# Kernel optimization log

Measured on AMD Instinct MI355X. Metric: run time of the kernel, lower is better.

Reference implementation:

```python
import jax, jax.numpy as jnp
import numpy as np

NEG = -1000000000.0
EPS = 1e-05

def setup_inputs() -> dict:
    key = jax.random.key(0)
    k1, k2, k3, k4, k5 = jax.random.split(key, 5)
    B, L, E, Q = 64, 2048, 512, 256
    encoded_vecs = jax.random.normal(k1, (B, L, E), dtype=jnp.float32)
    query = jax.random.normal(k2, (B, Q), dtype=jnp.float32)
    length = jax.random.randint(k3, (B,), 1, L + 1, dtype=jnp.int32)
    # Xavier-normal-ish params
    W1 = jax.random.normal(k4, (E + Q, E), dtype=jnp.float32) * jnp.sqrt(2.0 / (E + Q + E))
    b1 = jnp.zeros((E,), dtype=jnp.float32)
    v = jax.random.normal(k5, (E,), dtype=jnp.float32) * jnp.sqrt(2.0 / (E + 1))
    return {"encoded_vecs": encoded_vecs, "query": query, "length": length,
            "W1": W1, "b1": b1, "v": v}

def reference(encoded_vecs, query, length, W1, b1, v):
    B, L, E = encoded_vecs.shape
    # broadcast 2D query over the length dim (repeat in torch code)
    q = jnp.broadcast_to(query[:, None, :], (B, L, query.shape[-1]))
    h = jnp.concatenate([encoded_vecs, q], axis=2)            # [B, L, E+Q]
    u = jnp.tanh(jnp.einsum('blc,ce->ble', h, W1) + b1)       # [B, L, E]
    logits = jnp.einsum('ble,e->bl', u, v)                    # [B, L]
    # masked softmax (faithful to masked_softmax in source)
    mask = (jnp.arange(L)[None, :] < length[:, None])         # [B, L] bool
    masked_logits = jnp.where(mask, logits, NEG)
    max_logits = jnp.max(masked_logits, axis=1, keepdims=True)
    exps = jnp.exp(masked_logits - max_logits) * mask.astype(logits.dtype)
    attention = exps / (jnp.sum(exps, axis=1, keepdims=True) + EPS)  # [B, L]
    context = jnp.einsum('bl,ble->be', attention, encoded_vecs)      # [B, E]
    return (context, attention)
```

## Files before the change

kernel.cpp:

```cpp
#include <hip/hip_runtime.h>

typedef __attribute__((ext_vector_type(4))) float float4v;
typedef __attribute__((ext_vector_type(2))) float float2v;
typedef __attribute__((ext_vector_type(8))) short short8;
typedef __attribute__((ext_vector_type(4))) float f32x4;

#define NEGV (-1000000000.0f)

#define MTOT (64 * 2048)

__device__ __forceinline__ unsigned short f2bf(float f) {
    unsigned int u = __float_as_uint(f);
    u += 0x7fffu + ((u >> 16) & 1u);
    return (unsigned short)(u >> 16);
}

__device__ __forceinline__ void gload_lds16(const void* g, void* l) {
    __builtin_amdgcn_global_load_lds(
        (__attribute__((address_space(1))) unsigned int*)(unsigned long long)(g),
        (__attribute__((address_space(3))) unsigned int*)(unsigned int)(unsigned long long)(l),
        16, 0, 0);
}

__global__ __launch_bounds__(256)
void prep_wt_kernel(const float* __restrict__ W1, unsigned short* __restrict__ Wt) {
    __shared__ float t[32][33];
    int bx = blockIdx.x & 15;
    int by = blockIdx.x >> 4;
    int tx = threadIdx.x & 31;
    int ty = threadIdx.x >> 5;
    #pragma unroll
    for (int i = 0; i < 4; ++i)
        t[ty + 8 * i][tx] = W1[(bx * 32 + ty + 8 * i) * 512 + by * 32 + tx];
    __syncthreads();
    #pragma unroll
    for (int i = 0; i < 4; ++i)
        Wt[(by * 32 + ty + 8 * i) * 512 + bx * 32 + tx] = f2bf(t[tx][ty + 8 * i]);
}

__global__ void prep_qc_kernel(const float* __restrict__ query, const float* __restrict__ W1,
                               const float* __restrict__ b1, float* __restrict__ qc) {
    int b = blockIdx.x;
    int e = threadIdx.x;
    float acc0 = b1[e];
    float acc1 = b1[e + 256];
    const float* w = W1 + 512 * 512;
    #pragma unroll 8
    for (int q = 0; q < 256; ++q) {
        float qv = query[b * 256 + q];
        acc0 += qv * w[q * 512 + e];
        acc1 += qv * w[q * 512 + e + 256];
    }
    qc[b * 512 + e] = acc0;
    qc[b * 512 + e + 256] = acc1;
}

__global__ __launch_bounds__(256)
void prep_enc_kernel(const float* __restrict__ enc, const int* __restrict__ length,
                     unsigned short* __restrict__ Ab) {
    int bm = blockIdx.x;
    int b = bm >> 4;
    if ((bm & 15) * 128 >= length[b]) return;
    long base = (long)bm * 128 * 512;
    const float* src = enc + base;
    unsigned short* dst = Ab + base;
    int tid = threadIdx.x;
    #pragma unroll 4
    for (int i = 0; i < 32; ++i) {
        long idx = (long)(i * 256 + tid) * 8;
        float4v a = *(const float4v*)(src + idx);
        float4v c = *(const float4v*)(src + idx + 4);
        union { unsigned short u[8]; short8 s; } o;
        o.u[0] = f2bf(a[0]); o.u[1] = f2bf(a[1]); o.u[2] = f2bf(a[2]); o.u[3] = f2bf(a[3]);
        o.u[4] = f2bf(c[0]); o.u[5] = f2bf(c[1]); o.u[6] = f2bf(c[2]); o.u[7] = f2bf(c[3]);
        *(short8*)(dst + idx) = o.s;
    }
}

__global__ void build_wl_kernel(const int* __restrict__ length, int* __restrict__ wl,
                                int* __restrict__ meta) {
    int bm = blockIdx.x * 256 + threadIdx.x;
    int b = bm >> 4;
    if ((bm & 15) * 128 < length[b]) {
        int idx = atomicAdd(&meta[0], 1);
        wl[idx] = bm;
    }
}

__global__ __launch_bounds__(512)
void gemm_logits_kernel(const unsigned short* __restrict__ Ab,
                        const unsigned short* __restrict__ Wt,
                        const float* __restrict__ qc,
                        const float* __restrict__ v,
                        const int* __restrict__ wl,
                        int* __restrict__ meta,
                        float* __restrict__ part)
{
    __shared__ unsigned short As[3 * 128 * 64];
    __shared__ unsigned short Bs[3 * 256 * 64];
    __shared__ int s_t;

    int tid = threadIdx.x;
    int lane = tid & 63;
    int w = tid >> 6;
    int wm = w >> 2, wn = w & 3;

    int aoffs[2], boffs[4];
    int asrc[2], bsrc[4];
    #pragma unroll
    for (int i = 0; i < 2; ++i) {
        int off = (w * 2 + i) * 1024 + lane * 16;
        int r = off >> 7, kb = off & 127;
        aoffs[i] = off;
        asrc[i] = r * 1024 + (kb ^ ((r & 7) << 4));
    }
    #pragma unroll
    for (int i = 0; i < 4; ++i) {
        int off = (w * 4 + i) * 1024 + lane * 16;
        int r = off >> 7, kb = off & 127;
        boffs[i] = off;
        bsrc[i] = r * 1024 + (kb ^ ((r & 7) << 4));
    }

    int aoff[4][2], boff[4][2];
    int kbase = (lane >> 4) * 16;
    #pragma unroll
    for (int mi = 0; mi < 4; ++mi) {
        int ar = wm * 64 + (lane & 15) + mi * 16;
        #pragma unroll
        for (int kk = 0; kk < 2; ++kk)
            aoff[mi][kk] = ar * 128 + ((kk * 64 + kbase) ^ ((ar & 7) << 4));
    }
    #pragma unroll
    for (int ni = 0; ni < 4; ++ni) {
        int br = wn * 64 + (lane & 15) + ni * 16;
        #pragma unroll
        for (int kk = 0; kk < 2; ++kk)
            boff[ni][kk] = br * 128 + ((kk * 64 + kbase) ^ ((br & 7) << 4));
    }

    int nw = meta[0] * 2;

    for (;;) {
        if (tid == 0) s_t = atomicAdd(&meta[1], 1);
        __syncthreads();
        int t = s_t;
        if (t >= nw) break;
        int bm = wl[t >> 1];
        int bn = t & 1;
        int b = bm >> 4;
        long row0 = (long)bm * 128;
        int col0 = bn * 256;

        const char* gA = (const char*)Ab + row0 * 1024;
        const char* gB = (const char*)Wt + (long)col0 * 1024;

        f32x4 acc[4][4] = {};

#define STAGE(t_, sI) do {                                                   \
    char* la_ = (char*)As + (sI) * 16384;                                    \
    char* lb_ = (char*)Bs + (sI) * 32768;                                    \
    gload_lds16(gA + asrc[0] + (t_) * 128, la_ + aoffs[0]);                  \
    gload_lds16(gA + asrc[1] + (t_) * 128, la_ + aoffs[1]);                  \
    gload_lds16(gB + bsrc[0] + (t_) * 128, lb_ + boffs[0]);                  \
    gload_lds16(gB + bsrc[1] + (t_) * 128, lb_ + boffs[1]);                  \
    gload_lds16(gB + bsrc[2] + (t_) * 128, lb_ + boffs[2]);                  \
    gload_lds16(gB + bsrc[3] + (t_) * 128, lb_ + boffs[3]);                  \
} while (0)

#define KCOMP(sC) do {                                                       \
    const char* as_ = (const char*)As + (sC) * 16384;                        \
    const char* bs_ = (const char*)Bs + (sC) * 32768;                        \
    _Pragma("unroll")                                                        \
    for (int kk = 0; kk < 2; ++kk) {                                         \
        short8 af_[4];                                                       \
        _Pragma("unroll")                                                    \
        for (int mi = 0; mi < 4; ++mi)                                       \
            af_[mi] = *(const short8*)(as_ + aoff[mi][kk]);                  \
        _Pragma("unroll")                                                    \
        for (int ni = 0; ni < 4; ++ni) {                                     \
            short8 bf_ = *(const short8*)(bs_ + boff[ni][kk]);               \
            _Pragma("unroll")                                                \
            for (int mi = 0; mi < 4; ++mi)                                   \
                acc[mi][ni] = __builtin_amdgcn_mfma_f32_16x16x32_bf16(af_[mi], bf_, acc[mi][ni], 0, 0, 0); \
        }                                                                    \
    }                                                                        \
} while (0)

#define KITER(t_, stg_, sI_, sC_, VM_) do {                                  \
    STAGE(stg_, sI_);                                                        \
    asm volatile("s_waitcnt vmcnt(" #VM_ ")" ::: "memory");                  \
    __builtin_amdgcn_s_barrier();                                            \
    asm volatile("" ::: "memory");                                           \
    KCOMP(sC_);                                                              \
    asm volatile("" ::: "memory");                                           \
    __builtin_amdgcn_s_barrier();                                            \
} while (0)

        STAGE(0, 0);
        STAGE(1, 1);
        KITER(0, 2, 2, 0, 12);
        KITER(1, 3, 0, 1, 12);
        KITER(2, 4, 1, 2, 12);
        KITER(3, 5, 2, 0, 12);
        KITER(4, 6, 0, 1, 12);
        KITER(5, 7, 1, 2, 12);
        asm volatile("s_waitcnt vmcnt(6)" ::: "memory");
        __builtin_amdgcn_s_barrier();
        asm volatile("" ::: "memory");
        KCOMP(0);
        asm volatile("" ::: "memory");
        __builtin_amdgcn_s_barrier();
        asm volatile("s_waitcnt vmcnt(0)" ::: "memory");
        __builtin_amdgcn_s_barrier();
        asm volatile("" ::: "memory");
        KCOMP(1);

        const float* qcb = qc + b * 512;
        float vcol[4], qcol[4];
        #pragma unroll
        for (int ni = 0; ni < 4; ++ni) {
            int c = col0 + wn * 64 + ni * 16 + (lane & 15);
            vcol[ni] = v[c];
            qcol[ni] = qcb[c];
        }
        float* pslice = part + (bn * 4 + wn) * MTOT + row0;
        int rbase = wm * 64 + 4 * (lane >> 4);
        #pragma unroll
        for (int mi = 0; mi < 4; ++mi) {
            #pragma unroll
            for (int j2 = 0; j2 < 4; ++j2) {
                float s = 0.f;
                #pragma unroll
                for (int ni = 0; ni < 4; ++ni) {
                    float xx = acc[mi][ni][j2] + qcol[ni];
                    float e2 = __expf(2.0f * xx);
                    float tt = 1.0f - 2.0f * __builtin_amdgcn_rcpf(e2 + 1.0f);
                    s += tt * vcol[ni];
                }
                s += __shfl_xor(s, 1);
                s += __shfl_xor(s, 2);
                s += __shfl_xor(s, 4);
                s += __shfl_xor(s, 8);
                if ((lane & 15) == 0)
                    pslice[rbase + mi * 16 + j2] = s;
            }
        }
    }
}

__global__ void softmax_kernel(const float* __restrict__ part, const int* __restrict__ length,
                               float* __restrict__ att, float* __restrict__ ctx) {
    int b = blockIdx.x;
    int len = length[b];
    int tid = threadIdx.x;
    int lane = tid & 63, wv = tid >> 6;
    const float* p0 = part + b * 2048;
    float* ab = att + b * 2048;

    ctx[b * 512 + tid] = 0.f;
    ctx[b * 512 + 256 + tid] = 0.f;

    float vals[8];
    float mymax = -3.402823466e38f;
    #pragma unroll
    for (int i = 0; i < 8; ++i) {
        int l = tid + i * 256;
        float xv = NEGV;
        if (l < len) {
            xv = 0.f;
            #pragma unroll
            for (int s = 0; s < 8; ++s)
                xv += p0[s * MTOT + l];
        }
        vals[i] = xv;
        mymax = fmaxf(mymax, xv);
    }
    #pragma unroll
    for (int m = 32; m; m >>= 1) mymax = fmaxf(mymax, __shfl_xor(mymax, m));
    __shared__ float sm[4];
    if (lane == 0) sm[wv] = mymax;
    __syncthreads();
    float bmax = fmaxf(fmaxf(sm[0], sm[1]), fmaxf(sm[2], sm[3]));

    float mysum = 0.f;
    #pragma unroll
    for (int i = 0; i < 8; ++i) {
        int l = tid + i * 256;
        float e = (l < len) ? __expf(vals[i] - bmax) : 0.f;
        vals[i] = e;
        mysum += e;
    }
    #pragma unroll
    for (int m = 32; m; m >>= 1) mysum += __shfl_xor(mysum, m);
    __shared__ float ss[4];
    if (lane == 0) ss[wv] = mysum;
    __syncthreads();
    float tot = ss[0] + ss[1] + ss[2] + ss[3];
    float inv = 1.0f / (tot + 1e-5f);
    #pragma unroll
    for (int i = 0; i < 8; ++i) {
        int l = tid + i * 256;
        ab[l] = vals[i] * inv;
    }
}

__global__ void ctx_kernel(const float* __restrict__ att, const unsigned short* __restrict__ Ab,
                           const int* __restrict__ length, float* __restrict__ ctx) {
    int b = blockIdx.x;
    int lc = blockIdx.y;
    int len = length[b];
    int l0 = lc * 128;
    if (l0 >= len) return;
    int lim = len - l0;
    if (lim > 128) lim = 128;

    int t = threadIdx.x;
    const float* ab = att + b * 2048 + l0;
    const unsigned short* eb = Ab + ((long)(b * 2048 + l0)) * 512 + t * 2;
    float c0 = 0.f, c1 = 0.f;
    #pragma unroll 4
    for (int l = 0; l < lim; ++l) {
        float a = ab[l];
        unsigned int wv = *(const unsigned int*)(eb);
        eb += 512;
        c0 += a * __uint_as_float(wv << 16);
        c1 += a * __uint_as_float(wv & 0xffff0000u);
    }
    atomicAdd(&ctx[b * 512 + 2 * t], c0);
    atomicAdd(&ctx[b * 512 + 2 * t + 1], c1);
}

extern "C" void kernel_launch(void* const* d_in, const int* in_sizes, int n_in,
                              void* d_out, int out_size, void* d_ws, size_t ws_size,
                              hipStream_t stream) {
    const float* enc    = (const float*)d_in[0];
    const float* query  = (const float*)d_in[1];
    const int*   length = (const int*)d_in[2];
    const float* W1     = (const float*)d_in[3];
    const float* b1     = (const float*)d_in[4];
    const float* v      = (const float*)d_in[5];

    float* out = (float*)d_out;
    float* ctx = out;
    float* att = out + 64 * 512;

    char* ws = (char*)d_ws;
    float* part        = (float*)ws;
    float* qc          = (float*)(ws + 8L * MTOT * 4);
    unsigned short* Wt = (unsigned short*)(ws + 8L * MTOT * 4 + 64 * 512 * 4);
    int* wl            = (int*)(ws + 8L * MTOT * 4 + 64 * 512 * 4 + 512 * 1024);
    int* meta          = (int*)(ws + 8L * MTOT * 4 + 64 * 512 * 4 + 512 * 1024 + 4096);
    unsigned short* Ab = (unsigned short*)(ws + 8L * MTOT * 4 + 64 * 512 * 4 + 512 * 1024 + 8192);

    hipMemsetAsync(meta, 0, 8, stream);
    prep_wt_kernel<<<256, 256, 0, stream>>>(W1, Wt);
    prep_qc_kernel<<<64, 256, 0, stream>>>(query, W1, b1, qc);
    build_wl_kernel<<<4, 256, 0, stream>>>(length, wl, meta);
    prep_enc_kernel<<<1024, 256, 0, stream>>>(enc, length, Ab);

    gemm_logits_kernel<<<256, 512, 0, stream>>>(Ab, Wt, qc, v, wl, meta, part);

    softmax_kernel<<<64, 256, 0, stream>>>(part, length, att, ctx);

    dim3 g3(64, 16);
    ctx_kernel<<<g3, 256, 0, stream>>>(att, Ab, length, ctx);
}
```

Measured before the change: 155.6 us.

## Interleave split stage loads with MFMA halves, add setprio, prefetch next tile index

Measured after the change: 155.5 us. No clear change (-0.0%).

```diff
diff --git a/kernel.cpp b/kernel.cpp
--- a/kernel.cpp
+++ b/kernel.cpp
@@ -141,11 +141,11 @@
 
     int nw = meta[0] * 2;
 
-    for (;;) {
-        if (tid == 0) s_t = atomicAdd(&meta[1], 1);
-        __syncthreads();
-        int t = s_t;
-        if (t >= nw) break;
+    if (tid == 0) s_t = atomicAdd(&meta[1], 1);
+    __syncthreads();
+    int t = s_t;
+
+    while (t < nw) {
         int bm = wl[t >> 1];
         int bn = t & 1;
         int b = bm >> 4;
@@ -157,64 +157,77 @@
 
         f32x4 acc[4][4] = {};
 
-#define STAGE(t_, sI) do {                                                   \
+#define STAGE_A(t_, sI) do {                                                 \
     char* la_ = (char*)As + (sI) * 16384;                                    \
     char* lb_ = (char*)Bs + (sI) * 32768;                                    \
     gload_lds16(gA + asrc[0] + (t_) * 128, la_ + aoffs[0]);                  \
     gload_lds16(gA + asrc[1] + (t_) * 128, la_ + aoffs[1]);                  \
     gload_lds16(gB + bsrc[0] + (t_) * 128, lb_ + boffs[0]);                  \
     gload_lds16(gB + bsrc[1] + (t_) * 128, lb_ + boffs[1]);                  \
+} while (0)
+
+#define STAGE_B(t_, sI) do {                                                 \
+    char* lb_ = (char*)Bs + (sI) * 32768;                                    \
     gload_lds16(gB + bsrc[2] + (t_) * 128, lb_ + boffs[2]);                  \
     gload_lds16(gB + bsrc[3] + (t_) * 128, lb_ + boffs[3]);                  \
 } while (0)
 
-#define KCOMP(sC) do {                                                       \
+#define KCOMP_K(sC, kk) do {                                                 \
     const char* as_ = (const char*)As + (sC) * 16384;                        \
     const char* bs_ = (const char*)Bs + (sC) * 32768;                        \
+    short8 af_[4];                                                           \
     _Pragma("unroll")                                                        \
-    for (int kk = 0; kk < 2; ++kk) {                                         \
-        short8 af_[4];                                                       \
+    for (int mi = 0; mi < 4; ++mi)                                           \
+        af_[mi] = *(const short8*)(as_ + aoff[mi][kk]);                      \
+    _Pragma("unroll")                                                        \
+    for (int ni = 0; ni < 4; ++ni) {                                         \
+        short8 bf_ = *(const short8*)(bs_ + boff[ni][kk]);                   \
         _Pragma("unroll")                                                    \
         for (int mi = 0; mi < 4; ++mi)                                       \
-            af_[mi] = *(const short8*)(as_ + aoff[mi][kk]);                  \
-        _Pragma("unroll")                                                    \
-        for (int ni = 0; ni < 4; ++ni) {                                     \
-            short8 bf_ = *(const short8*)(bs_ + boff[ni][kk]);               \
-            _Pragma("unroll")                                                \
-            for (int mi = 0; mi < 4; ++mi)                                   \
-                acc[mi][ni] = __builtin_amdgcn_mfma_f32_16x16x32_bf16(af_[mi], bf_, acc[mi][ni], 0, 0, 0); \
-        }                                                                    \
+            acc[mi][ni] = __builtin_amdgcn_mfma_f32_16x16x32_bf16(af_[mi], bf_, acc[mi][ni], 0, 0, 0); \
     }                                                                        \
 } while (0)
 
-#define KITER(t_, stg_, sI_, sC_, VM_) do {                                  \
-    STAGE(stg_, sI_);                                                        \
-    asm volatile("s_waitcnt vmcnt(" #VM_ ")" ::: "memory");                  \
+#define KITER(t_, stg_, sI_, sC_) do {                                       \
+    STAGE_A(stg_, sI_);                                                      \
+    asm volatile("s_waitcnt vmcnt(10)" ::: "memory");                        \
     __builtin_amdgcn_s_barrier();                                            \
     asm volatile("" ::: "memory");                                           \
-    KCOMP(sC_);                                                              \
+    __builtin_amdgcn_s_setprio(1);                                           \
+    KCOMP_K(sC_, 0);                                                         \
+    __builtin_amdgcn_s_setprio(0);                                           \
+    STAGE_B(stg_, sI_);                                                      \
+    __builtin_amdgcn_s_setprio(1);                                           \
+    KCOMP_K(sC_, 1);                                                         \
+    __builtin_amdgcn_s_setprio(0);                                           \
     asm volatile("" ::: "memory");                                           \
     __builtin_amdgcn_s_barrier();                                            \
 } while (0)
 
-        STAGE(0, 0);
-        STAGE(1, 1);
-        KITER(0, 2, 2, 0, 12);
-        KITER(1, 3, 0, 1, 12);
-        KITER(2, 4, 1, 2, 12);
-        KITER(3, 5, 2, 0, 12);
-        KITER(4, 6, 0, 1, 12);
-        KITER(5, 7, 1, 2, 12);
+        STAGE_A(0, 0); STAGE_B(0, 0);
+        STAGE_A(1, 1); STAGE_B(1, 1);
+        KITER(0, 2, 2, 0);
+        KITER(1, 3, 0, 1);
+        KITER(2, 4, 1, 2);
+        KITER(3, 5, 2, 0);
+        KITER(4, 6, 0, 1);
+        KITER(5, 7, 1, 2);
         asm volatile("s_waitcnt vmcnt(6)" ::: "memory");
         __builtin_amdgcn_s_barrier();
         asm volatile("" ::: "memory");
-        KCOMP(0);
+        __builtin_amdgcn_s_setprio(1);
+        KCOMP_K(0, 0);
+        KCOMP_K(0, 1);
+        __builtin_amdgcn_s_setprio(0);
         asm volatile("" ::: "memory");
         __builtin_amdgcn_s_barrier();
         asm volatile("s_waitcnt vmcnt(0)" ::: "memory");
         __builtin_amdgcn_s_barrier();
         asm volatile("" ::: "memory");
-        KCOMP(1);
+        KCOMP_K(1, 0);
+        KCOMP_K(1, 1);
+
+        if (tid == 0) s_t = atomicAdd(&meta[1], 1);
 
         const float* qcb = qc + b * 512;
         float vcol[4], qcol[4];
@@ -246,6 +259,8 @@
                     pslice[rbase + mi * 16 + j2] = s;
             }
         }
+        __syncthreads();
+        t = s_t;
     }
 }
 
```

## Enlarge GEMM M-tile to 256 rows with K=32 stages and interleaved loads

Applied to the files above, without the earlier changes.

Result: slower. 160.3 us (+3.0%).

```diff
diff --git a/kernel.cpp b/kernel.cpp
--- a/kernel.cpp
+++ b/kernel.cpp
@@ -80,8 +80,8 @@
 __global__ void build_wl_kernel(const int* __restrict__ length, int* __restrict__ wl,
                                 int* __restrict__ meta) {
     int bm = blockIdx.x * 256 + threadIdx.x;
-    int b = bm >> 4;
-    if ((bm & 15) * 128 < length[b]) {
+    int b = bm >> 3;
+    if ((bm & 7) * 256 < length[b]) {
         int idx = atomicAdd(&meta[0], 1);
         wl[idx] = bm;
     }
@@ -96,8 +96,8 @@
                         int* __restrict__ meta,
                         float* __restrict__ part)
 {
-    __shared__ unsigned short As[3 * 128 * 64];
-    __shared__ unsigned short Bs[3 * 256 * 64];
+    __shared__ unsigned short As[3 * 256 * 32];
+    __shared__ unsigned short Bs[3 * 256 * 32];
     __shared__ int s_t;
 
     int tid = threadIdx.x;
@@ -105,116 +105,118 @@
     int w = tid >> 6;
     int wm = w >> 2, wn = w & 3;
 
-    int aoffs[2], boffs[4];
-    int asrc[2], bsrc[4];
+    int sA_off[2], sA_src[2];
     #pragma unroll
     for (int i = 0; i < 2; ++i) {
         int off = (w * 2 + i) * 1024 + lane * 16;
-        int r = off >> 7, kb = off & 127;
-        aoffs[i] = off;
-        asrc[i] = r * 1024 + (kb ^ ((r & 7) << 4));
-    }
-    #pragma unroll
-    for (int i = 0; i < 4; ++i) {
-        int off = (w * 4 + i) * 1024 + lane * 16;
-        int r = off >> 7, kb = off & 127;
-        boffs[i] = off;
-        bsrc[i] = r * 1024 + (kb ^ ((r & 7) << 4));
-    }
-
-    int aoff[4][2], boff[4][2];
+        int r = off >> 6, kb = off & 63;
+        sA_off[i] = off;
+        sA_src[i] = r * 1024 + (kb ^ (((r >> 1) & 3) << 4));
+    }
+
+    int aoff[2][4], boff[4];
     int kbase = (lane >> 4) * 16;
     #pragma unroll
-    for (int mi = 0; mi < 4; ++mi) {
-        int ar = wm * 64 + (lane & 15) + mi * 16;
+    for (int mh = 0; mh < 2; ++mh)
         #pragma unroll
-        for (int kk = 0; kk < 2; ++kk)
-            aoff[mi][kk] = ar * 128 + ((kk * 64 + kbase) ^ ((ar & 7) << 4));
-    }
+        for (int mi = 0; mi < 4; ++mi) {
+            int ar = wm * 128 + mh * 64 + mi * 16 + (lane & 15);
+            aoff[mh][mi] = ar * 64 + (kbase ^ (((ar >> 1) & 3) << 4));
+        }
     #pragma unroll
     for (int ni = 0; ni < 4; ++ni) {
-        int br = wn * 64 + (lane & 15) + ni * 16;
-        #pragma unroll
-        for (int kk = 0; kk < 2; ++kk)
-            boff[ni][kk] = br * 128 + ((kk * 64 + kbase) ^ ((br & 7) << 4));
+        int br = wn * 64 + ni * 16 + (lane & 15);
+        boff[ni] = br * 64 + (kbase ^ (((br >> 1) & 3) << 4));
     }
 
     int nw = meta[0] * 2;
 
-    for (;;) {
-        if (tid == 0) s_t = atomicAdd(&meta[1], 1);
-        __syncthreads();
-        int t = s_t;
-        if (t >= nw) break;
+    if (tid == 0) s_t = atomicAdd(&meta[1], 1);
+    __syncthreads();
+    int t = s_t;
+
+    while (t < nw) {
         int bm = wl[t >> 1];
         int bn = t & 1;
-        int b = bm >> 4;
-        long row0 = (long)bm * 128;
+        int b = bm >> 3;
+        long row0 = (long)bm * 256;
         int col0 = bn * 256;
 
         const char* gA = (const char*)Ab + row0 * 1024;
         const char* gB = (const char*)Wt + (long)col0 * 1024;
 
-        f32x4 acc[4][4] = {};
-
-#define STAGE(t_, sI) do {                                                   \
-    char* la_ = (char*)As + (sI) * 16384;                                    \
-    char* lb_ = (char*)Bs + (sI) * 32768;                                    \
-    gload_lds16(gA + asrc[0] + (t_) * 128, la_ + aoffs[0]);                  \
-    gload_lds16(gA + asrc[1] + (t_) * 128, la_ + aoffs[1]);                  \
-    gload_lds16(gB + bsrc[0] + (t_) * 128, lb_ + boffs[0]);                  \
-    gload_lds16(gB + bsrc[1] + (t_) * 128, lb_ + boffs[1]);                  \
-    gload_lds16(gB + bsrc[2] + (t_) * 128, lb_ + boffs[2]);                  \
-    gload_lds16(gB + bsrc[3] + (t_) * 128, lb_ + boffs[3]);                  \
+        f32x4 acc[8][4] = {};
+
+#define ISS_A(t_, sI) do {                                                   \
+    char* l_ = (char*)As + (sI) * 16384;                                     \
+    gload_lds16(gA + sA_src[0] + (t_) * 64, l_ + sA_off[0]);                 \
+    gload_lds16(gA + sA_src[1] + (t_) * 64, l_ + sA_off[1]);                 \
 } while (0)
 
-#define KCOMP(sC) do {                                                       \
-    const char* as_ = (const char*)As + (sC) * 16384;                        \
-    const char* bs_ = (const char*)Bs + (sC) * 32768;                        \
+#define ISS_B(t_, sI) do {                                                   \
+    char* l_ = (char*)Bs + (sI) * 16384;                                     \
+    gload_lds16(gB + sA_src[0] + (t_) * 64, l_ + sA_off[0]);                 \
+    gload_lds16(gB + sA_src[1] + (t_) * 64, l_ + sA_off[1]);                 \
+} while (0)
+
+#define MFMA_HALF(mh) do {                                                   \
     _Pragma("unroll")                                                        \
-    for (int kk = 0; kk < 2; ++kk) {                                         \
-        short8 af_[4];                                                       \
+    for (int mi = 0; mi < 4; ++mi)                                           \
         _Pragma("unroll")                                                    \
-        for (int mi = 0; mi < 4; ++mi)                                       \
-            af_[mi] = *(const short8*)(as_ + aoff[mi][kk]);                  \
-        _Pragma("unroll")                                                    \
-        for (int ni = 0; ni < 4; ++ni) {                                     \
-            short8 bf_ = *(const short8*)(bs_ + boff[ni][kk]);               \
-            _Pragma("unroll")                                                \
-            for (int mi = 0; mi < 4; ++mi)                                   \
-                acc[mi][ni] = __builtin_amdgcn_mfma_f32_16x16x32_bf16(af_[mi], bf_, acc[mi][ni], 0, 0, 0); \
-        }                                                                    \
-    }                                                                        \
+        for (int ni = 0; ni < 4; ++ni)                                       \
+            acc[(mh) * 4 + mi][ni] =                                         \
+                __builtin_amdgcn_mfma_f32_16x16x32_bf16(af_[mi], bf_[ni],    \
+                    acc[(mh) * 4 + mi][ni], 0, 0, 0);                        \
 } while (0)
 
-#define KITER(t_, stg_, sI_, sC_, VM_) do {                                  \
-    STAGE(stg_, sI_);                                                        \
-    asm volatile("s_waitcnt vmcnt(" #VM_ ")" ::: "memory");                  \
+#define KITER(t_, sC, sI, ISS, VM) do {                                      \
+    asm volatile("s_waitcnt vmcnt(" #VM ")" ::: "memory");                   \
     __builtin_amdgcn_s_barrier();                                            \
     asm volatile("" ::: "memory");                                           \
-    KCOMP(sC_);                                                              \
+    {                                                                        \
+        const char* as_ = (const char*)As + (sC) * 16384;                    \
+        const char* bs_ = (const char*)Bs + (sC) * 16384;                    \
+        short8 af_[4], bf_[4];                                               \
+        if (ISS) ISS_A((t_) + 2, sI);                                        \
+        _Pragma("unroll")                                                    \
+        for (int ni = 0; ni < 4; ++ni) bf_[ni] = *(const short8*)(bs_ + boff[ni]); \
+        _Pragma("unroll")                                                    \
+        for (int mi = 0; mi < 4; ++mi) af_[mi] = *(const short8*)(as_ + aoff[0][mi]); \
+        __builtin_amdgcn_s_setprio(1);                                       \
+        MFMA_HALF(0);                                                        \
+        __builtin_amdgcn_s_setprio(0);                                       \
+        if (ISS) ISS_B((t_) + 2, sI);                                        \
+        _Pragma("unroll")                                                    \
+        for (int mi = 0; mi < 4; ++mi) af_[mi] = *(const short8*)(as_ + aoff[1][mi]); \
+        __builtin_amdgcn_s_setprio(1);                                       \
+        MFMA_HALF(1);                                                        \
+        __builtin_amdgcn_s_setprio(0);                                       \
+    }                                                                        \
     asm volatile("" ::: "memory");                                           \
     __builtin_amdgcn_s_barrier();                                            \
 } while (0)
 
-        STAGE(0, 0);
-        STAGE(1, 1);
-        KITER(0, 2, 2, 0, 12);
-        KITER(1, 3, 0, 1, 12);
-        KITER(2, 4, 1, 2, 12);
-        KITER(3, 5, 2, 0, 12);
-        KITER(4, 6, 0, 1, 12);
-        KITER(5, 7, 1, 2, 12);
-        asm volatile("s_waitcnt vmcnt(6)" ::: "memory");
-        __builtin_amdgcn_s_barrier();
-        asm volatile("" ::: "memory");
-        KCOMP(0);
-        asm volatile("" ::: "memory");
-        __builtin_amdgcn_s_barrier();
-        asm volatile("s_waitcnt vmcnt(0)" ::: "memory");
-        __builtin_amdgcn_s_barrier();
-        asm volatile("" ::: "memory");
-        KCOMP(1);
+        ISS_A(0, 0); ISS_B(0, 0);
+        ISS_A(1, 1); ISS_B(1, 1);
+
+        KITER(0,  0, 2, 1, 4);
+        KITER(1,  1, 0, 1, 4);
+        KITER(2,  2, 1, 1, 4);
+        KITER(3,  0, 2, 1, 4);
+        KITER(4,  1, 0, 1, 4);
+        KITER(5,  2, 1, 1, 4);
+        KITER(6,  0, 2, 1, 4);
+        KITER(7,  1, 0, 1, 4);
+        KITER(8,  2, 1, 1, 4);
+        KITER(9,  0, 2, 1, 4);
+        KITER(10, 1, 0, 1, 4);
+        KITER(11, 2, 1, 1, 4);
+        KITER(12, 0, 2, 1, 4);
+        KITER(13, 1, 0, 1, 4);
+        KITER(14, 2, 0, 0, 4);
+        KITER(15, 0, 0, 0, 0);
+
+        if (tid == 0) s_t = atomicAdd(&meta[1], 1);
 
         const float* qcb = qc + b * 512;
         float vcol[4], qcol[4];
@@ -225,9 +227,8 @@
             qcol[ni] = qcb[c];
         }
         float* pslice = part + (bn * 4 + wn) * MTOT + row0;
-        int rbase = wm * 64 + 4 * (lane >> 4);
         #pragma unroll
-        for (int mi = 0; mi < 4; ++mi) {
+        for (int mi = 0; mi < 8; ++mi) {
             #pragma unroll
             for (int j2 = 0; j2 < 4; ++j2) {
                 float s = 0.f;
@@ -243,9 +244,11 @@
                 s += __shfl_xor(s, 4);
                 s += __shfl_xor(s, 8);
                 if ((lane & 15) == 0)
-                    pslice[rbase + mi * 16 + j2] = s;
+                    pslice[wm * 128 + mi * 16 + 4 * (lane >> 4) + j2] = s;
             }
         }
+        __syncthreads();
+        t = s_t;
     }
 }
 
@@ -356,7 +359,7 @@
     hipMemsetAsync(meta, 0, 8, stream);
     prep_wt_kernel<<<256, 256, 0, stream>>>(W1, Wt);
     prep_qc_kernel<<<64, 256, 0, stream>>>(query, W1, b1, qc);
-    build_wl_kernel<<<4, 256, 0, stream>>>(length, wl, meta);
+    build_wl_kernel<<<2, 256, 0, stream>>>(length, wl, meta);
     prep_enc_kernel<<<1024, 256, 0, stream>>>(enc, length, Ab);
 
     gemm_logits_kernel<<<256, 512, 0, stream>>>(Ab, Wt, qc, v, wl, meta, part);
```
